# Performance work log

Hardware: AMD Instinct MI355X
Metric: run time of the kernel (lower is better)

The kernel has to match this reference:

```python
import jax, jax.numpy as jnp
import numpy as np

B, NF, V, D, NI = 16384, 26, 100000, 16, 13
HID = [512, 256, 128, 64, 1]

def setup_inputs() -> dict:
    key = jax.random.key(0)
    ks = jax.random.split(key, 24)
    x_int = jax.random.normal(ks[0], (B, NI), dtype=jnp.float32)
    x_cat = jax.random.randint(ks[1], (B, NF), 0, V, dtype=jnp.int64)
    emb_tables = jax.random.normal(ks[2], (NF, V, D), dtype=jnp.float32) * 0.01
    lin_tables = jax.random.normal(ks[3], (NF, V, 1), dtype=jnp.float32) * 0.01
    W_num = jax.random.normal(ks[4], (NI, 1), dtype=jnp.float32) * 0.1
    b_num = jnp.zeros((1,), dtype=jnp.float32)
    bias = jnp.zeros((1,), dtype=jnp.float32)
    dims = [NF * D + NI] + HID  # 429 -> 512 -> 256 -> 128 -> 64 -> 1
    mlp = {}
    for li in range(5):
        fan_in = dims[li]
        mlp[f'W{li+1}'] = jax.random.normal(ks[5 + 2*li], (dims[li], dims[li+1]), dtype=jnp.float32) / np.sqrt(fan_in)
        mlp[f'b{li+1}'] = jnp.zeros((dims[li+1],), dtype=jnp.float32)
    return dict(x_int=x_int, x_cat=x_cat, emb_tables=emb_tables, lin_tables=lin_tables,
                W_num=W_num, b_num=b_num, bias=bias, **mlp)

def reference(x_int, x_cat, emb_tables, lin_tables, W_num, b_num, bias,
              W1, b1, W2, b2, W3, b3, W4, b4, W5, b5):
    feat_idx = jnp.arange(NF)[None, :]                 # [1, NF]
    emb = emb_tables[feat_idx, x_cat]                  # [B, NF, D] fused gather
    # FM second-order interaction
    sum_emb = jnp.sum(emb, axis=1)                     # [B, D]
    square_of_sum = sum_emb ** 2
    sum_of_square = jnp.sum(emb ** 2, axis=1)
    fm_score = 0.5 * jnp.sum(square_of_sum - sum_of_square, axis=1, keepdims=True)  # [B,1]
    # linear terms
    lin_cat_score = jnp.sum(lin_tables[feat_idx, x_cat], axis=1)  # [B,1]
    lin_num_score = x_int @ W_num + b_num                          # [B,1]
    # deep MLP (dropout is identity at inference)
    deep_in = jnp.concatenate([emb.reshape(emb.shape[0], -1), x_int], axis=1)  # [B, NF*D+NI]
    h = jax.nn.relu(deep_in @ W1 + b1)
    h = jax.nn.relu(h @ W2 + b2)
    h = jax.nn.relu(h @ W3 + b3)
    h = jax.nn.relu(h @ W4 + b4)
    deep_score = h @ W5 + b5                                       # [B,1]
    return bias + lin_cat_score + lin_num_score + fm_score + deep_score
```

## Files before the change

kernel.cpp:

```cpp
#include <hip/hip_runtime.h>
#include <hip/hip_bf16.h>
#include <stdint.h>

typedef __bf16 bf16x8 __attribute__((ext_vector_type(8)));
typedef __bf16 bf16x4 __attribute__((ext_vector_type(4)));
typedef float  f32x4  __attribute__((ext_vector_type(4)));

#define NROWS 16384
#define NFEAT 26
#define VOCAB 100000

template<int KPAD, int KREAL, int N, int NCT, int WS>
__device__ __forceinline__ void mlp_layer(const float* __restrict__ W,
                                          const float* __restrict__ bias,
                                          const __bf16* Ain, __bf16* Aout,
                                          int w, int lane) {
  constexpr int LDA = KPAD + 8, LDO = N + 8;
  const int lrow = lane & 15;
  const int kg = (lane >> 4) * 8;

  f32x4 acc[NCT][4];
  #pragma unroll
  for (int j = 0; j < NCT; ++j)
    #pragma unroll
    for (int m = 0; m < 4; ++m)
      #pragma unroll
      for (int i = 0; i < 4; ++i) acc[j][m][i] = 0.f;

  int col[NCT];
  #pragma unroll
  for (int j = 0; j < NCT; ++j) col[j] = (w + j * WS) * 16 + lrow;

  for (int k0 = 0; k0 < KREAL; k0 += 32) {
    bf16x8 af[4];
    #pragma unroll
    for (int m = 0; m < 4; ++m)
      af[m] = *(const bf16x8*)(Ain + (m * 16 + lrow) * LDA + k0 + kg);
    #pragma unroll
    for (int j = 0; j < NCT; ++j) {
      bf16x8 bw;
      #pragma unroll
      for (int i = 0; i < 8; ++i)
        bw[i] = (__bf16)W[(size_t)(k0 + kg + i) * N + col[j]];
      #pragma unroll
      for (int m = 0; m < 4; ++m)
        acc[j][m] = __builtin_amdgcn_mfma_f32_16x16x32_bf16(af[m], bw, acc[j][m], 0, 0, 0);
    }
  }

  const int rbase = (lane >> 4) * 4;
  #pragma unroll
  for (int j = 0; j < NCT; ++j) {
    float bv = bias[col[j]];
    #pragma unroll
    for (int m = 0; m < 4; ++m)
      #pragma unroll
      for (int i = 0; i < 4; ++i) {
        float v = acc[j][m][i] + bv;
        v = fmaxf(v, 0.f);
        Aout[(m * 16 + rbase + i) * LDO + col[j]] = (__bf16)v;
      }
  }
}

__global__ __launch_bounds__(1024) void k_fused(
    const float* __restrict__ x_int,
    const int*   __restrict__ x_cat,
    const float* __restrict__ emb,
    const float* __restrict__ lin,
    const float* __restrict__ W_num,
    const float* __restrict__ b_num,
    const float* __restrict__ bias0,
    const float* __restrict__ W1, const float* __restrict__ b1,
    const float* __restrict__ W2, const float* __restrict__ b2,
    const float* __restrict__ W3, const float* __restrict__ b3,
    const float* __restrict__ W4, const float* __restrict__ b4,
    const float* __restrict__ W5, const float* __restrict__ b5,
    float* __restrict__ out) {
  __shared__ __align__(16) char smem[125184];
  __bf16* A0 = (__bf16*)smem;
  __bf16* A1 = (__bf16*)(smem + 58368);
  int* s_idx = (int*)(smem + 58368);
  float* s_part = (float*)(smem + 124928);

  const int t = threadIdx.x;
  const int row0 = blockIdx.x * 64;
  const int w = t >> 6, lane = t & 63;
  const int lrow = lane & 15, kg = (lane >> 4) * 8;

  for (int i = t; i < 64 * NFEAT; i += 1024) {
    int r = i / NFEAT, f = i - r * NFEAT;
    s_idx[i] = x_cat[(size_t)(row0 + r) * NFEAT + f];
  }
  __syncthreads();

  const int r = t >> 4, d = t & 15;
  const int g = d >> 2, q = d & 3;

  float lin_s = 0.f;
  if (d < 13) {
    lin_s = lin[(size_t)d * VOCAB + s_idx[r * NFEAT + d]]
          + lin[(size_t)(d + 13) * VOCAB + s_idx[r * NFEAT + d + 13]]
          + x_int[(size_t)(row0 + r) * 13 + d] * W_num[d];
  }
  float xv[4] = {0.f, 0.f, 0.f, 0.f};
  if (d >= 8 && d < 12) {
    int base = (d - 8) * 4;
    #pragma unroll
    for (int i = 0; i < 4; ++i)
      if (base + i < 13) xv[i] = x_int[(size_t)(row0 + r) * 13 + base + i];
  }

  f32x4 acc[2][4];
  #pragma unroll
  for (int j = 0; j < 2; ++j)
    #pragma unroll
    for (int m = 0; m < 4; ++m)
      #pragma unroll
      for (int i = 0; i < 4; ++i) acc[j][m][i] = 0.f;
  const int colL1[2] = { w * 16 + lrow, (w + 16) * 16 + lrow };

  float fsum[4] = {0.f,0.f,0.f,0.f}, fsq[4] = {0.f,0.f,0.f,0.f};
  f32x4 cur;
  {
    int idx = s_idx[r * NFEAT + g];
    cur = *(const f32x4*)(emb + ((size_t)g * VOCAB + idx) * 16 + q * 4);
  }

  #pragma unroll
  for (int c = 0; c < 7; ++c) {
    f32x4 nxt;
    if (c < 6) {
      int fc = 4 * (c + 1) + g;
      if (fc < NFEAT) {
        int idx = s_idx[r * NFEAT + fc];
        nxt = *(const f32x4*)(emb + ((size_t)fc * VOCAB + idx) * 16 + q * 4);
      }
    }
    const int colbase = c * 64 + g * 16 + q * 4;
    if (4 * c + g < NFEAT) {
      bf16x4 pk;
      #pragma unroll
      for (int i = 0; i < 4; ++i) {
        fsum[i] += cur[i]; fsq[i] += cur[i] * cur[i];
        pk[i] = (__bf16)cur[i];
      }
      *(bf16x4*)(A0 + r * 456 + colbase) = pk;
    } else {
      bf16x4 pk;
      #pragma unroll
      for (int i = 0; i < 4; ++i) pk[i] = (__bf16)xv[i];
      *(bf16x4*)(A0 + r * 456 + colbase) = pk;
    }
    asm volatile("s_waitcnt lgkmcnt(0)" ::: "memory");
    __builtin_amdgcn_s_barrier();
    asm volatile("" ::: "memory");
    #pragma unroll
    for (int ks = 0; ks < 2; ++ks) {
      const int k0 = c * 64 + ks * 32;
      bf16x8 af[4];
      #pragma unroll
      for (int m = 0; m < 4; ++m)
        af[m] = *(const bf16x8*)(A0 + (m * 16 + lrow) * 456 + k0 + kg);
      #pragma unroll
      for (int j = 0; j < 2; ++j) {
        bf16x8 bw;
        #pragma unroll
        for (int i = 0; i < 8; ++i) {
          int k = k0 + kg + i;
          float v;
          if (c < 6) v = W1[(size_t)k * 512 + colL1[j]];
          else       v = (k < 429) ? W1[(size_t)k * 512 + colL1[j]] : 0.f;
          bw[i] = (__bf16)v;
        }
        #pragma unroll
        for (int m = 0; m < 4; ++m)
          acc[j][m] = __builtin_amdgcn_mfma_f32_16x16x32_bf16(af[m], bw, acc[j][m], 0, 0, 0);
      }
    }
    cur = nxt;
  }

  {
    const int rbase = (lane >> 4) * 4;
    #pragma unroll
    for (int j = 0; j < 2; ++j) {
      float bv = b1[colL1[j]];
      #pragma unroll
      for (int m = 0; m < 4; ++m)
        #pragma unroll
        for (int i = 0; i < 4; ++i) {
          float v = acc[j][m][i] + bv;
          v = fmaxf(v, 0.f);
          A1[(m * 16 + rbase + i) * 520 + colL1[j]] = (__bf16)v;
        }
    }
  }

  {
    #pragma unroll
    for (int i = 0; i < 4; ++i) {
      fsum[i] += __shfl_xor(fsum[i], 4); fsq[i] += __shfl_xor(fsq[i], 4);
      fsum[i] += __shfl_xor(fsum[i], 8); fsq[i] += __shfl_xor(fsq[i], 8);
    }
    float fmq = 0.f;
    #pragma unroll
    for (int i = 0; i < 4; ++i) fmq += fsum[i] * fsum[i] - fsq[i];
    fmq += __shfl_xor(fmq, 1);
    fmq += __shfl_xor(fmq, 2);
    float linred = lin_s;
    #pragma unroll
    for (int off = 1; off < 16; off <<= 1) linred += __shfl_xor(linred, off, 16);
    if (d == 0) s_part[r] = 0.5f * fmq + linred + bias0[0] + b_num[0];
  }
  __syncthreads();

  mlp_layer<512, 512, 256, 1, 16>(W2, b2, A1, A0, w, lane);
  __syncthreads();
  if (w < 8) mlp_layer<256, 256, 128, 1, 8>(W3, b3, A0, A1, w, lane);
  __syncthreads();
  if (w < 4) mlp_layer<128, 128, 64, 1, 4>(W4, b4, A1, A0, w, lane);
  __syncthreads();

  {
    const int rr = t >> 4, gg = t & 15;
    float s = 0.f;
    #pragma unroll
    for (int i = 0; i < 4; ++i)
      s += (float)A0[rr * 72 + gg * 4 + i] * W5[gg * 4 + i];
    #pragma unroll
    for (int off = 1; off < 16; off <<= 1) s += __shfl_xor(s, off, 16);
    if (gg == 0) out[row0 + rr] = s + b5[0] + s_part[rr];
  }
}

extern "C" void kernel_launch(void* const* d_in, const int* in_sizes, int n_in,
                              void* d_out, int out_size, void* d_ws, size_t ws_size,
                              hipStream_t stream) {
  const float* x_int = (const float*)d_in[0];
  const int*   x_cat = (const int*)d_in[1];
  const float* emb   = (const float*)d_in[2];
  const float* lin   = (const float*)d_in[3];
  const float* W_num = (const float*)d_in[4];
  const float* b_num = (const float*)d_in[5];
  const float* bias  = (const float*)d_in[6];
  const float* W1 = (const float*)d_in[7];  const float* b1 = (const float*)d_in[8];
  const float* W2 = (const float*)d_in[9];  const float* b2 = (const float*)d_in[10];
  const float* W3 = (const float*)d_in[11]; const float* b3 = (const float*)d_in[12];
  const float* W4 = (const float*)d_in[13]; const float* b4 = (const float*)d_in[14];
  const float* W5 = (const float*)d_in[15]; const float* b5 = (const float*)d_in[16];
  float* out = (float*)d_out;

  k_fused<<<NROWS / 64, 1024, 0, stream>>>(x_int, x_cat, emb, lin, W_num, b_num, bias,
                                           W1, b1, W2, b2, W3, b3, W4, b4, W5, b5,
                                           out);
}
```

Measured before the change: 44.17 us.

## Pre-transpose MLP weights to bf16 and shrink blocks to 32 rows

Adds a small kernel that runs on every call and transposes W1-W4 into K-contiguous, zero-padded bf16 copies in the workspace. The fused kernel can then load each MFMA B fragment with one 16-byte load, replacing eight strided fp32 loads with conversion. The fused kernel also moves from 64-row, 1024-thread blocks to 32-row, 512-thread blocks with half the LDS, allowing several blocks per CU. It deepens the embedding prefetch to two stages and rebalances column tiles per wave. The cost is an extra launch plus the transpose traffic on every call, and each block now reuses every weight fragment across fewer rows.

```diff
diff --git a/kernel.cpp b/kernel.cpp
--- a/kernel.cpp
+++ b/kernel.cpp
@@ -10,20 +10,57 @@
 #define NFEAT 26
 #define VOCAB 100000
 
-template<int KPAD, int KREAL, int N, int NCT, int WS>
-__device__ __forceinline__ void mlp_layer(const float* __restrict__ W,
+__device__ __forceinline__ void bar_lgkm() {
+  asm volatile("s_waitcnt lgkmcnt(0)" ::: "memory");
+  __builtin_amdgcn_s_barrier();
+  asm volatile("" ::: "memory");
+}
+
+__device__ __forceinline__ void transpose_tile(const float* __restrict__ W,
+                                               __bf16* __restrict__ Wt,
+                                               int K, int N, int Kpad,
+                                               int kt, int nt, int t) {
+  __shared__ float tile[32][33];
+  const int tx = t & 31, ty = t >> 5;
+  const int k0 = kt * 32, n0 = nt * 32;
+  #pragma unroll
+  for (int j = 0; j < 4; ++j) {
+    int k = k0 + ty + j * 8;
+    tile[ty + j * 8][tx] = (k < K) ? W[(size_t)k * N + n0 + tx] : 0.f;
+  }
+  __syncthreads();
+  #pragma unroll
+  for (int j = 0; j < 4; ++j) {
+    int n = n0 + ty + j * 8;
+    Wt[(size_t)n * Kpad + k0 + tx] = (__bf16)tile[tx][ty + j * 8];
+  }
+}
+
+__global__ __launch_bounds__(256) void k_convAll(
+    const float* __restrict__ W1, const float* __restrict__ W2,
+    const float* __restrict__ W3, const float* __restrict__ W4,
+    __bf16* __restrict__ Wt1, __bf16* __restrict__ Wt2,
+    __bf16* __restrict__ Wt3, __bf16* __restrict__ Wt4) {
+  const int b = blockIdx.x, t = threadIdx.x;
+  if (b < 224)       { int i = b;        transpose_tile(W1, Wt1, 429, 512, 448, i % 14, i / 14, t); }
+  else if (b < 352)  { int i = b - 224;  transpose_tile(W2, Wt2, 512, 256, 512, i % 16, i / 16, t); }
+  else if (b < 384)  { int i = b - 352;  transpose_tile(W3, Wt3, 256, 128, 256, i % 8,  i / 8,  t); }
+  else               { int i = b - 384;  transpose_tile(W4, Wt4, 128,  64, 128, i % 4,  i / 4,  t); }
+}
+
+template<int MT, int LDA, int KP, int N, int NCT, int WS, int LDO>
+__device__ __forceinline__ void mlp_layer(const __bf16* __restrict__ Wt,
                                           const float* __restrict__ bias,
                                           const __bf16* Ain, __bf16* Aout,
                                           int w, int lane) {
-  constexpr int LDA = KPAD + 8, LDO = N + 8;
   const int lrow = lane & 15;
   const int kg = (lane >> 4) * 8;
 
-  f32x4 acc[NCT][4];
+  f32x4 acc[NCT][MT];
   #pragma unroll
   for (int j = 0; j < NCT; ++j)
     #pragma unroll
-    for (int m = 0; m < 4; ++m)
+    for (int m = 0; m < MT; ++m)
       #pragma unroll
       for (int i = 0; i < 4; ++i) acc[j][m][i] = 0.f;
 
@@ -31,19 +68,16 @@
   #pragma unroll
   for (int j = 0; j < NCT; ++j) col[j] = (w + j * WS) * 16 + lrow;
 
-  for (int k0 = 0; k0 < KREAL; k0 += 32) {
-    bf16x8 af[4];
-    #pragma unroll
-    for (int m = 0; m < 4; ++m)
+  for (int k0 = 0; k0 < KP; k0 += 32) {
+    bf16x8 af[MT];
+    #pragma unroll
+    for (int m = 0; m < MT; ++m)
       af[m] = *(const bf16x8*)(Ain + (m * 16 + lrow) * LDA + k0 + kg);
     #pragma unroll
     for (int j = 0; j < NCT; ++j) {
-      bf16x8 bw;
-      #pragma unroll
-      for (int i = 0; i < 8; ++i)
-        bw[i] = (__bf16)W[(size_t)(k0 + kg + i) * N + col[j]];
-      #pragma unroll
-      for (int m = 0; m < 4; ++m)
+      bf16x8 bw = *(const bf16x8*)(Wt + (size_t)col[j] * KP + k0 + kg);
+      #pragma unroll
+      for (int m = 0; m < MT; ++m)
         acc[j][m] = __builtin_amdgcn_mfma_f32_16x16x32_bf16(af[m], bw, acc[j][m], 0, 0, 0);
     }
   }
@@ -53,7 +87,7 @@
   for (int j = 0; j < NCT; ++j) {
     float bv = bias[col[j]];
     #pragma unroll
-    for (int m = 0; m < 4; ++m)
+    for (int m = 0; m < MT; ++m)
       #pragma unroll
       for (int i = 0; i < 4; ++i) {
         float v = acc[j][m][i] + bv;
@@ -63,7 +97,7 @@
   }
 }
 
-__global__ __launch_bounds__(1024) void k_fused(
+__global__ __launch_bounds__(512, 4) void k_fused(
     const float* __restrict__ x_int,
     const int*   __restrict__ x_cat,
     const float* __restrict__ emb,
@@ -71,28 +105,29 @@
     const float* __restrict__ W_num,
     const float* __restrict__ b_num,
     const float* __restrict__ bias0,
-    const float* __restrict__ W1, const float* __restrict__ b1,
-    const float* __restrict__ W2, const float* __restrict__ b2,
-    const float* __restrict__ W3, const float* __restrict__ b3,
-    const float* __restrict__ W4, const float* __restrict__ b4,
+    const __bf16* __restrict__ Wt1, const float* __restrict__ b1,
+    const __bf16* __restrict__ Wt2, const float* __restrict__ b2,
+    const __bf16* __restrict__ Wt3, const float* __restrict__ b3,
+    const __bf16* __restrict__ Wt4, const float* __restrict__ b4,
     const float* __restrict__ W5, const float* __restrict__ b5,
     float* __restrict__ out) {
-  __shared__ __align__(16) char smem[125184];
+  __shared__ __align__(16) char smem[62592];
   __bf16* A0 = (__bf16*)smem;
-  __bf16* A1 = (__bf16*)(smem + 58368);
-  int* s_idx = (int*)(smem + 58368);
-  float* s_part = (float*)(smem + 124928);
+  __bf16* A1 = (__bf16*)(smem + 29184);
+  int* s_idx = (int*)(smem + 29184);
+  float* s_part = (float*)(smem + 62464);
 
   const int t = threadIdx.x;
-  const int row0 = blockIdx.x * 64;
+  const int row0 = blockIdx.x * 32;
   const int w = t >> 6, lane = t & 63;
   const int lrow = lane & 15, kg = (lane >> 4) * 8;
 
-  for (int i = t; i < 64 * NFEAT; i += 1024) {
+  #pragma unroll
+  for (int i = t; i < 32 * NFEAT; i += 512) {
     int r = i / NFEAT, f = i - r * NFEAT;
     s_idx[i] = x_cat[(size_t)(row0 + r) * NFEAT + f];
   }
-  __syncthreads();
+  bar_lgkm();
 
   const int r = t >> 4, d = t & 15;
   const int g = d >> 2, q = d & 3;
@@ -111,27 +146,33 @@
       if (base + i < 13) xv[i] = x_int[(size_t)(row0 + r) * 13 + base + i];
   }
 
-  f32x4 acc[2][4];
-  #pragma unroll
-  for (int j = 0; j < 2; ++j)
-    #pragma unroll
-    for (int m = 0; m < 4; ++m)
+  f32x4 acc[4][2];
+  #pragma unroll
+  for (int j = 0; j < 4; ++j)
+    #pragma unroll
+    for (int m = 0; m < 2; ++m)
       #pragma unroll
       for (int i = 0; i < 4; ++i) acc[j][m][i] = 0.f;
-  const int colL1[2] = { w * 16 + lrow, (w + 16) * 16 + lrow };
+  int col1[4];
+  #pragma unroll
+  for (int j = 0; j < 4; ++j) col1[j] = (w + j * 8) * 16 + lrow;
 
   float fsum[4] = {0.f,0.f,0.f,0.f}, fsq[4] = {0.f,0.f,0.f,0.f};
-  f32x4 cur;
+  f32x4 p0, p1;
   {
     int idx = s_idx[r * NFEAT + g];
-    cur = *(const f32x4*)(emb + ((size_t)g * VOCAB + idx) * 16 + q * 4);
+    p0 = *(const f32x4*)(emb + ((size_t)g * VOCAB + idx) * 16 + q * 4);
+  }
+  {
+    int idx = s_idx[r * NFEAT + 4 + g];
+    p1 = *(const f32x4*)(emb + ((size_t)(4 + g) * VOCAB + idx) * 16 + q * 4);
   }
 
   #pragma unroll
   for (int c = 0; c < 7; ++c) {
     f32x4 nxt;
-    if (c < 6) {
-      int fc = 4 * (c + 1) + g;
+    if (c < 5) {
+      int fc = 4 * (c + 2) + g;
       if (fc < NFEAT) {
         int idx = s_idx[r * NFEAT + fc];
         nxt = *(const f32x4*)(emb + ((size_t)fc * VOCAB + idx) * 16 + q * 4);
@@ -142,8 +183,8 @@
       bf16x4 pk;
       #pragma unroll
       for (int i = 0; i < 4; ++i) {
-        fsum[i] += cur[i]; fsq[i] += cur[i] * cur[i];
-        pk[i] = (__bf16)cur[i];
+        fsum[i] += p0[i]; fsq[i] += p0[i] * p0[i];
+        pk[i] = (__bf16)p0[i];
       }
       *(bf16x4*)(A0 + r * 456 + colbase) = pk;
     } else {
@@ -152,47 +193,37 @@
       for (int i = 0; i < 4; ++i) pk[i] = (__bf16)xv[i];
       *(bf16x4*)(A0 + r * 456 + colbase) = pk;
     }
-    asm volatile("s_waitcnt lgkmcnt(0)" ::: "memory");
-    __builtin_amdgcn_s_barrier();
-    asm volatile("" ::: "memory");
+    bar_lgkm();
     #pragma unroll
     for (int ks = 0; ks < 2; ++ks) {
       const int k0 = c * 64 + ks * 32;
-      bf16x8 af[4];
-      #pragma unroll
-      for (int m = 0; m < 4; ++m)
+      bf16x8 af[2];
+      #pragma unroll
+      for (int m = 0; m < 2; ++m)
         af[m] = *(const bf16x8*)(A0 + (m * 16 + lrow) * 456 + k0 + kg);
       #pragma unroll
-      for (int j = 0; j < 2; ++j) {
-        bf16x8 bw;
+      for (int j = 0; j < 4; ++j) {
+        bf16x8 bw = *(const bf16x8*)(Wt1 + (size_t)col1[j] * 448 + k0 + kg);
         #pragma unroll
-        for (int i = 0; i < 8; ++i) {
-          int k = k0 + kg + i;
-          float v;
-          if (c < 6) v = W1[(size_t)k * 512 + colL1[j]];
-          else       v = (k < 429) ? W1[(size_t)k * 512 + colL1[j]] : 0.f;
-          bw[i] = (__bf16)v;
-        }
-        #pragma unroll
-        for (int m = 0; m < 4; ++m)
+        for (int m = 0; m < 2; ++m)
           acc[j][m] = __builtin_amdgcn_mfma_f32_16x16x32_bf16(af[m], bw, acc[j][m], 0, 0, 0);
       }
     }
-    cur = nxt;
+    p0 = p1; p1 = nxt;
   }
 
   {
     const int rbase = (lane >> 4) * 4;
     #pragma unroll
-    for (int j = 0; j < 2; ++j) {
-      float bv = b1[colL1[j]];
-      #pragma unroll
-      for (int m = 0; m < 4; ++m)
+    for (int j = 0; j < 4; ++j) {
+      float bv = b1[col1[j]];
+      #pragma unroll
+      for (int m = 0; m < 2; ++m)
         #pragma unroll
         for (int i = 0; i < 4; ++i) {
           float v = acc[j][m][i] + bv;
           v = fmaxf(v, 0.f);
-          A1[(m * 16 + rbase + i) * 520 + colL1[j]] = (__bf16)v;
+          A1[(m * 16 + rbase + i) * 520 + col1[j]] = (__bf16)v;
         }
     }
   }
@@ -213,14 +244,14 @@
     for (int off = 1; off < 16; off <<= 1) linred += __shfl_xor(linred, off, 16);
     if (d == 0) s_part[r] = 0.5f * fmq + linred + bias0[0] + b_num[0];
   }
-  __syncthreads();
-
-  mlp_layer<512, 512, 256, 1, 16>(W2, b2, A1, A0, w, lane);
-  __syncthreads();
-  if (w < 8) mlp_layer<256, 256, 128, 1, 8>(W3, b3, A0, A1, w, lane);
-  __syncthreads();
-  if (w < 4) mlp_layer<128, 128, 64, 1, 4>(W4, b4, A1, A0, w, lane);
-  __syncthreads();
+  bar_lgkm();
+
+  mlp_layer<2, 520, 512, 256, 2, 8, 264>(Wt2, b2, A1, A0, w, lane);
+  bar_lgkm();
+  mlp_layer<2, 264, 256, 128, 1, 8, 136>(Wt3, b3, A0, A1, w, lane);
+  bar_lgkm();
+  if (w < 4) mlp_layer<2, 136, 128, 64, 1, 4, 72>(Wt4, b4, A1, A0, w, lane);
+  bar_lgkm();
 
   {
     const int rr = t >> 4, gg = t & 15;
@@ -251,7 +282,15 @@
   const float* W5 = (const float*)d_in[15]; const float* b5 = (const float*)d_in[16];
   float* out = (float*)d_out;
 
-  k_fused<<<NROWS / 64, 1024, 0, stream>>>(x_int, x_cat, emb, lin, W_num, b_num, bias,
-                                           W1, b1, W2, b2, W3, b3, W4, b4, W5, b5,
-                                           out);
-}
+  char* ws = (char*)d_ws;
+  __bf16* Wt1 = (__bf16*)(ws);
+  __bf16* Wt2 = (__bf16*)(ws + 458752);
+  __bf16* Wt3 = (__bf16*)(ws + 720896);
+  __bf16* Wt4 = (__bf16*)(ws + 786432);
+
+  k_convAll<<<392, 256, 0, stream>>>(W1, W2, W3, W4, Wt1, Wt2, Wt3, Wt4);
+
+  k_fused<<<NROWS / 32, 512, 0, stream>>>(x_int, x_cat, emb, lin, W_num, b_num, bias,
+                                          Wt1, b1, Wt2, b2, Wt3, b3, Wt4, b4, W5, b5,
+                                          out);
+}
```

Result: slower. 67.33 us (+52.4%).
